# Kernel optimization log

Measured on AMD Instinct MI355X. Metric: run time of the kernel, lower is better.

## Reference

```python
import jax, jax.numpy as jnp
import numpy as np

# DH-SFNN: 2 dendritic LIF layers (denri, no tanh, reset-by-subtraction) + leaky readout integrator.
GAMMA = 0.5   # surrogate gradient scale
LENS = 0.5    # surrogate gradient width
VTH = 1.0     # spike threshold
DT = 1.0

@jax.custom_vjp
def spike_fn(x):
    # Heaviside forward, Gaussian surrogate backward (act_fun_adp)
    return (x > 0.0).astype(x.dtype)

def _spike_fwd(x):
    return spike_fn(x), x

def _spike_bwd(x, g):
    sg = GAMMA * jnp.exp(-x * x / (2.0 * LENS * LENS)) / (jnp.sqrt(2.0 * jnp.pi) * LENS)
    return (g * sg,)

spike_fn.defvjp(_spike_fwd, _spike_bwd)

B, T, IN, H, O, K = 256, 250, 700, 256, 20, 4  # batch, time, in_dim, hidden, out_dim, branch
WARMUP = 10


def _branch_mask(rng, out_dim, in_dim, k):
    # Each neuron's k branches see a disjoint random partition of the inputs.
    m = np.zeros((out_dim * k, in_dim), np.float32)
    step = in_dim // k
    for i in range(out_dim):
        perm = rng.permutation(in_dim)
        for j in range(k):
            m[i * k + j, perm[j * step:(j + 1) * step]] = 1.0
    return m


def setup_inputs() -> dict:
    key = jax.random.key(0)
    ks = jax.random.split(key, 12)
    rng = np.random.default_rng(0)
    s1 = 1.0 / np.sqrt(IN)
    s2 = 1.0 / np.sqrt(H)
    # branch-masked dense weights (apply_mask() already baked in)
    W1 = jax.random.uniform(ks[0], (H * K, IN), minval=-s1, maxval=s1) * jnp.asarray(_branch_mask(rng, H, IN, K))
    b1 = jax.random.uniform(ks[1], (H * K,), minval=-s1, maxval=s1)
    tau_n1 = jax.random.uniform(ks[2], (H, K), minval=2.0, maxval=6.0)
    tau_m1 = jax.random.uniform(ks[3], (H,), minval=0.0, maxval=4.0)
    W2 = jax.random.uniform(ks[4], (H * K, H), minval=-s2, maxval=s2) * jnp.asarray(_branch_mask(rng, H, H, K))
    b2 = jax.random.uniform(ks[5], (H * K,), minval=-s2, maxval=s2)
    tau_n2 = jax.random.uniform(ks[6], (H, K), minval=2.0, maxval=6.0)
    tau_m2 = jax.random.uniform(ks[7], (H,), minval=0.0, maxval=4.0)
    Wr = jax.random.uniform(ks[8], (O, H), minval=-s2, maxval=s2)
    br = jax.random.uniform(ks[9], (O,), minval=-s2, maxval=s2)
    tau_mr = jax.random.uniform(ks[10], (O,), minval=0.0, maxval=4.0)
    # sparse binary spike train input (SHD-like)
    x = (jax.random.uniform(ks[11], (B, T, IN)) < 0.1).astype(jnp.float32)
    return dict(x=x, W1=W1, b1=b1, tau_n1=tau_n1, tau_m1=tau_m1,
                W2=W2, b2=b2, tau_n2=tau_n2, tau_m2=tau_m2,
                Wr=Wr, br=br, tau_mr=tau_mr, warmup=WARMUP)


def reference(x, W1, b1, tau_n1, tau_m1, W2, b2, tau_n2, tau_m2, Wr, br, tau_mr, warmup):
    Bb, Tt, _ = x.shape
    beta1 = jax.nn.sigmoid(tau_n1)   # [H,K] dendritic decay
    alpha1 = jax.nn.sigmoid(tau_m1)  # [H]   soma decay
    beta2 = jax.nn.sigmoid(tau_n2)
    alpha2 = jax.nn.sigmoid(tau_m2)
    alphar = jax.nn.sigmoid(tau_mr)  # [O]

    def dense_branch(inp, W, b):
        return (inp @ W.T + b).reshape(inp.shape[0], -1, K)  # [B,H,K]

    def step(carry, xt):
        d1, m1, s1, d2, m2, s2, mr, acc, t = carry
        # layer 1: dendritic filtering then LIF with soft reset
        d1 = beta1 * d1 + (1.0 - beta1) * dense_branch(xt, W1, b1)
        m1 = m1 * alpha1 + (1.0 - alpha1) * DT * d1.sum(-1) - VTH * s1
        s1 = spike_fn(m1 - VTH)
        # layer 2
        d2 = beta2 * d2 + (1.0 - beta2) * dense_branch(s1, W2, b2)
        m2 = m2 * alpha2 + (1.0 - alpha2) * DT * d2.sum(-1) - VTH * s2
        s2 = spike_fn(m2 - VTH)
        # leaky readout integrator
        mr = mr * alphar + (1.0 - alphar) * (s2 @ Wr.T + br)
        acc = acc + jnp.where(t >= warmup, mr, jnp.zeros_like(mr))
        return (d1, m1, s1, d2, m2, s2, mr, acc, t + 1), None

    z = lambda *s: jnp.zeros(s, x.dtype)
    carry0 = (z(Bb, H, K), z(Bb, H), z(Bb, H),
              z(Bb, H, K), z(Bb, H), z(Bb, H),
              z(Bb, O), z(Bb, O), jnp.int32(0))
    carry, _ = jax.lax.scan(step, carry0, jnp.moveaxis(x, 1, 0))
    acc = carry[7]
    return acc / (Tt - warmup)  # readout_mode == 'mean'
```

## Files before the change

### kernel.cpp

```cpp
#include <hip/hip_runtime.h>
#include <hip/hip_bf16.h>

typedef unsigned short us16;
typedef unsigned int u32;

#define B_   256
#define T_   250
#define IN_  700
#define KP_  704
#define H_   256
#define O_   20
#define HK_  1024
#define NPAIR_ (B_ * T_)
#define LDP_ 40
#define CP_  132

typedef __attribute__((ext_vector_type(8))) short short8;
typedef __attribute__((ext_vector_type(4))) float f32x4;

__device__ __forceinline__ float bfbits(unsigned int lo16) {
    union { unsigned int i; float f; } v; v.i = lo16 << 16; return v.f;
}
__device__ __forceinline__ float bflo(unsigned int u) {
    union { unsigned int i; float f; } v; v.i = u << 16; return v.f;
}
__device__ __forceinline__ float bfhi(unsigned int u) {
    union { unsigned int i; float f; } v; v.i = u & 0xffff0000u; return v.f;
}
__device__ __forceinline__ us16 f2bfu(float f) {
    __hip_bfloat16 h = __float2bfloat16(f);
    union { __hip_bfloat16 h; us16 u; } c; c.h = h; return c.u;
}
__device__ __forceinline__ float sigm(float x) { return 1.0f / (1.0f + expf(-x)); }
__device__ __forceinline__ int rfl(int v) { return __builtin_amdgcn_readfirstlane(v); }

__device__ __forceinline__ bool detect_bf16(const us16* __restrict__ taun) {
    int ok = 0;
#pragma unroll
    for (int i = 0; i < 8; i += 2) ok += ((taun[i] >> 8) == 0x40) ? 1 : 0;
    return ok == 4;
}
__device__ __forceinline__ float ldany(const void* __restrict__ p, long i, bool isb) {
    return isb ? bfbits(((const us16*)p)[i]) : ((const float*)p)[i];
}

__device__ __forceinline__ void async_cp16(const us16* g, us16* l) {
    __builtin_amdgcn_global_load_lds(
        (const __attribute__((address_space(1))) u32*)g,
        (__attribute__((address_space(3))) u32*)l, 16, 0, 0);
}

__global__ __launch_bounds__(256) void cvt_rows2(
    const void* __restrict__ xin, const void* __restrict__ w1in,
    us16* __restrict__ xout, us16* __restrict__ w1out,
    const us16* __restrict__ taun) {
    const bool isb = detect_bf16(taun);
    const int r = blockIdx.x * 4 + (threadIdx.x >> 6);
    const int l = threadIdx.x & 63;
    const void* in; us16* out; long ibase, obase;
    if (r < NPAIR_) {
        in = xin;  out = xout;  ibase = (long)r * IN_; obase = (long)r * KP_;
    } else {
        const int r2 = r - NPAIR_;
        if (r2 >= HK_) return;
        in = w1in; out = w1out; ibase = (long)r2 * IN_; obase = (long)r2 * KP_;
    }
    for (int c = l; c < 176; c += 64) {
        uint2 o;
        if (c < 175) {
            if (isb) {
                o = *(const uint2*)((const us16*)in + ibase + 4 * c);
            } else {
                float4 f = *(const float4*)((const float*)in + ibase + 4 * c);
                o.x = (u32)f2bfu(f.x) | ((u32)f2bfu(f.y) << 16);
                o.y = (u32)f2bfu(f.z) | ((u32)f2bfu(f.w) << 16);
            }
        } else { o.x = 0u; o.y = 0u; }
        *(uint2*)(out + obase + 4 * c) = o;
    }
}

__global__ void transpose_to_bf16(const void* __restrict__ in, us16* __restrict__ out,
                                  int R, int C, const us16* __restrict__ taun) {
    const bool isb = detect_bf16(taun);
    __shared__ us16 tile[32][33];
    int c0 = blockIdx.x * 32, r0 = blockIdx.y * 32;
    int tx = threadIdx.x, ty = threadIdx.y;
#pragma unroll
    for (int j = 0; j < 32; j += 8) {
        int r = r0 + ty + j, c = c0 + tx;
        if (r < R && c < C) tile[ty + j][tx] = f2bfu(ldany(in, (long)r * C + c, isb));
    }
    __syncthreads();
#pragma unroll
    for (int j = 0; j < 32; j += 8) {
        int c = c0 + ty + j, r = r0 + tx;
        if (c < C && r < R) out[(long)c * R + r] = tile[tx][ty + j];
    }
}

__global__ __launch_bounds__(256) void gemm_bf(
    const us16* __restrict__ Xb, const us16* __restrict__ W1b,
    us16* __restrict__ Apre)
{
    __shared__ __align__(16) us16 smem[32768];

    const int L  = blockIdx.x;
    const int mt = (L & 7) + ((L >> 6) << 3);
    const int nt = (L >> 3) & 7;
    if (mt >= NPAIR_ / 128) return;
    const int m0 = mt * 128, n0 = nt * 128;

    const int tid  = threadIdx.x;
    const int lane = tid & 63;
    const int w    = tid >> 6;
    const int wr   = w >> 1, wc = w & 1;
    const int l16  = lane & 15, quad = lane >> 4;

    const int rr    = lane >> 3;
    const int ccsw  = ((lane & 7) ^ rr) * 8;
    const us16* xg[4]; const us16* wg[4];
    int asl[4], bsl[4];
#pragma unroll
    for (int i = 0; i < 4; ++i) {
        const int blkrow = (w * 4 + i) * 8;
        xg[i]  = Xb  + (long)(m0 + blkrow + rr) * KP_ + ccsw;
        wg[i]  = W1b + (long)(n0 + blkrow + rr) * KP_ + ccsw;
        asl[i] = (w * 4 + i) * 512;
        bsl[i] = 8192 + (w * 4 + i) * 512;
    }

    f32x4 acc[4][4];
#pragma unroll
    for (int i = 0; i < 4; ++i)
#pragma unroll
        for (int j = 0; j < 4; ++j) acc[i][j] = (f32x4){0.f, 0.f, 0.f, 0.f};

    const int sw = l16 & 7;
    int aoff0[4], aoff1[4], boff0[4], boff1[4];
#pragma unroll
    for (int i = 0; i < 4; ++i) {
        const int ar = wr * 64 + i * 16 + l16;
        const int br = wc * 64 + i * 16 + l16;
        aoff0[i] = ar * 64 + ((quad ^ sw) << 3);
        aoff1[i] = ar * 64 + (((quad + 4) ^ sw) << 3);
        boff0[i] = 8192 + br * 64 + ((quad ^ sw) << 3);
        boff1[i] = 8192 + br * 64 + (((quad + 4) ^ sw) << 3);
    }

#pragma unroll
    for (int i = 0; i < 4; ++i) async_cp16(xg[i], smem + asl[i]);
#pragma unroll
    for (int i = 0; i < 4; ++i) async_cp16(wg[i], smem + bsl[i]);
    __syncthreads();

    for (int s = 0; s < 11; ++s) {
        const int cur = (s & 1) * 16384;
        const int nxt = 16384 - cur;
        if (s + 1 < 11) {
            const int kb = (s + 1) * 64;
#pragma unroll
            for (int i = 0; i < 4; ++i) async_cp16(xg[i] + kb, smem + nxt + asl[i]);
#pragma unroll
            for (int i = 0; i < 4; ++i) async_cp16(wg[i] + kb, smem + nxt + bsl[i]);
        }

        short8 af[4][2], bfv[4][2];
#pragma unroll
        for (int i = 0; i < 4; ++i) {
            af[i][0]  = *(const short8*)(smem + cur + aoff0[i]);
            af[i][1]  = *(const short8*)(smem + cur + aoff1[i]);
            bfv[i][0] = *(const short8*)(smem + cur + boff0[i]);
            bfv[i][1] = *(const short8*)(smem + cur + boff1[i]);
        }
#pragma unroll
        for (int h = 0; h < 2; ++h)
#pragma unroll
            for (int i = 0; i < 4; ++i)
#pragma unroll
                for (int j = 0; j < 4; ++j)
                    acc[i][j] = __builtin_amdgcn_mfma_f32_16x16x32_bf16(
                        af[i][h], bfv[j][h], acc[i][j], 0, 0, 0);

        __syncthreads();
    }

#pragma unroll
    for (int i = 0; i < 4; ++i)
#pragma unroll
        for (int j = 0; j < 4; ++j)
#pragma unroll
            for (int r = 0; r < 4; ++r)
                smem[(wr * 64 + i * 16 + quad * 4 + r) * CP_ +
                     (wc * 64 + j * 16 + l16)] = f2bfu(acc[i][j][r]);
    __syncthreads();
    for (int r2 = 0; r2 < 32; ++r2) {
        const int row = w * 32 + r2;
        const u32 v = *(const u32*)(smem + row * CP_ + lane * 2);
        *(u32*)(Apre + (long)(m0 + row) * HK_ + n0 + lane * 2) = v;
    }
}

__global__ __launch_bounds__(256) void dhsfnn_pc(
    const us16* __restrict__ Apre,
    const void* __restrict__ b1,  const void* __restrict__ tau_n1,
    const void* __restrict__ tau_m1,
    const void* __restrict__ b2,  const void* __restrict__ tau_n2,
    const void* __restrict__ tau_m2,
    const void* __restrict__ Wr,  const void* __restrict__ br,
    const void* __restrict__ tau_mr,
    const us16* __restrict__ W2T,
    const int* __restrict__ warmup_p,
    void* __restrict__ out)
{
    __shared__ __align__(16) us16 ring[2][16 * HK_];

    const int tid  = threadIdx.x;
    const int lane = tid & 63;
    const int w    = tid >> 6;
    const int b    = blockIdx.x;
    const bool isb = detect_bf16((const us16*)tau_n1);
    const int wu   = *warmup_p;

    const us16* apb = Apre + (long)b * T_ * HK_;

    for (int seg = w; seg < 32; seg += 4)
        async_cp16(apb + seg * 512 + lane * 8, ring[0] + seg * 512);

    float be1[16], cb1[16], ce1[16], be2[16], cb2[16], ce2[16], d1[16], d2[16];
#pragma unroll
    for (int e = 0; e < 16; ++e) {
        const long gi = (e < 8) ? ((long)lane * 8 + e) : (512 + (long)lane * 8 + e - 8);
        const float t1 = sigm(ldany(tau_n1, gi, isb));
        be1[e] = t1; ce1[e] = 1.f - t1; cb1[e] = ce1[e] * ldany(b1, gi, isb);
        const float t2 = sigm(ldany(tau_n2, gi, isb));
        be2[e] = t2; ce2[e] = 1.f - t2; cb2[e] = ce2[e] * ldany(b2, gi, isb);
        d1[e] = 0.f; d2[e] = 0.f;
    }
    float al1[4], al2[4], m1[4], s1[4], m2[4], s2[4];
#pragma unroll
    for (int j = 0; j < 4; ++j) {
        const int n = (j < 2) ? (2 * lane + j) : (128 + 2 * lane + (j - 2));
        al1[j] = sigm(ldany(tau_m1, n, isb));
        al2[j] = sigm(ldany(tau_m2, n, isb));
        m1[j] = 0.f; s1[j] = 0.f; m2[j] = 0.f; s2[j] = 0.f;
    }
    float alr = 0.f, brv = 0.f;
    if (lane < O_) { alr = sigm(ldany(tau_mr, lane, isb)); brv = ldany(br, lane, isb); }
    float mrv = 0.f, accO = 0.f;

    __syncthreads();

    for (int c = 0; c < 16; ++c) {
        const int t0 = c * 16;
        const int nst = (T_ - t0 < 16) ? (T_ - t0) : 16;

        if (w != 0) {
            if (c + 1 < 16) {
                const int t1c  = (c + 1) * 16;
                const int nseg = ((T_ - t1c < 16) ? (T_ - t1c) : 16) * 2;
                const us16* src = apb + (long)t1c * HK_;
                us16* dst = ring[(c + 1) & 1];
                for (int seg = w - 1; seg < nseg; seg += 3)
                    async_cp16(src + seg * 512 + lane * 8, dst + seg * 512);
            }
        } else {
            const us16* rb = ring[c & 1];
            uint4 cLo = *(const uint4*)(rb + lane * 8);
            uint4 cHi = *(const uint4*)(rb + 512 + lane * 8);
            for (int q = 0; q < nst; ++q) {
                uint4 nLo = cLo, nHi = cHi;
                if (q + 1 < nst) {
                    nLo = *(const uint4*)(rb + (q + 1) * HK_ + lane * 8);
                    nHi = *(const uint4*)(rb + (q + 1) * HK_ + 512 + lane * 8);
                }
                const int t = t0 + q;
                float a[16];
                a[0]=bflo(cLo.x);  a[1]=bfhi(cLo.x);  a[2]=bflo(cLo.y);  a[3]=bfhi(cLo.y);
                a[4]=bflo(cLo.z);  a[5]=bfhi(cLo.z);  a[6]=bflo(cLo.w);  a[7]=bfhi(cLo.w);
                a[8]=bflo(cHi.x);  a[9]=bfhi(cHi.x);  a[10]=bflo(cHi.y); a[11]=bfhi(cHi.y);
                a[12]=bflo(cHi.z); a[13]=bfhi(cHi.z); a[14]=bflo(cHi.w); a[15]=bfhi(cHi.w);

#pragma unroll
                for (int e = 0; e < 16; ++e)
                    d1[e] = be1[e] * d1[e] + cb1[e] + ce1[e] * a[e];

                unsigned long long bal1[4];
#pragma unroll
                for (int j = 0; j < 4; ++j) {
                    const float s = (d1[j*4+0] + d1[j*4+1]) + (d1[j*4+2] + d1[j*4+3]);
                    m1[j] = m1[j] * al1[j] + (1.f - al1[j]) * s - s1[j];
                    s1[j] = (m1[j] > 1.0f) ? 1.f : 0.f;
                    bal1[j] = __ballot(s1[j] > 0.f);
                }

                if ((bal1[0] | bal1[1] | bal1[2] | bal1[3]) != 0ull) {
                    float g[16];
#pragma unroll
                    for (int e = 0; e < 16; ++e) g[e] = 0.f;
                    for (int j2 = 0; j2 < 4; ++j2) {
                        unsigned long long mm = bal1[j2];
                        while (mm) {
                            const int i = __ffsll(mm) - 1; mm &= mm - 1;
                            const int n = (j2 < 2) ? (2 * i + j2) : (128 + 2 * i + (j2 - 2));
                            const us16* wv = W2T + ((long)n << 10);
                            const uint4 wl = *(const uint4*)(wv + lane * 8);
                            const uint4 wh = *(const uint4*)(wv + 512 + lane * 8);
                            g[0]+=bflo(wl.x);  g[1]+=bfhi(wl.x);  g[2]+=bflo(wl.y);  g[3]+=bfhi(wl.y);
                            g[4]+=bflo(wl.z);  g[5]+=bfhi(wl.z);  g[6]+=bflo(wl.w);  g[7]+=bfhi(wl.w);
                            g[8]+=bflo(wh.x);  g[9]+=bfhi(wh.x);  g[10]+=bflo(wh.y); g[11]+=bfhi(wh.y);
                            g[12]+=bflo(wh.z); g[13]+=bfhi(wh.z); g[14]+=bflo(wh.w); g[15]+=bfhi(wh.w);
                        }
                    }
#pragma unroll
                    for (int e = 0; e < 16; ++e)
                        d2[e] = be2[e] * d2[e] + cb2[e] + ce2[e] * g[e];
                } else {
#pragma unroll
                    for (int e = 0; e < 16; ++e)
                        d2[e] = be2[e] * d2[e] + cb2[e];
                }

                unsigned long long bal2[4];
#pragma unroll
                for (int j = 0; j < 4; ++j) {
                    const float s = (d2[j*4+0] + d2[j*4+1]) + (d2[j*4+2] + d2[j*4+3]);
                    m2[j] = m2[j] * al2[j] + (1.f - al2[j]) * s - s2[j];
                    s2[j] = (m2[j] > 1.0f) ? 1.f : 0.f;
                    bal2[j] = __ballot(s2[j] > 0.f);
                }

                if (lane < O_) {
                    float sum = brv;
                    if ((bal2[0] | bal2[1] | bal2[2] | bal2[3]) != 0ull) {
                        for (int j2 = 0; j2 < 4; ++j2) {
                            unsigned long long mm = bal2[j2];
                            while (mm) {
                                const int i = __ffsll(mm) - 1; mm &= mm - 1;
                                const int n = (j2 < 2) ? (2 * i + j2) : (128 + 2 * i + (j2 - 2));
                                sum += ldany(Wr, (long)lane * H_ + n, isb);
                            }
                        }
                    }
                    mrv = alr * mrv + (1.f - alr) * sum;
                    if (t >= wu) accO += mrv;
                }
                cLo = nLo; cHi = nHi;
            }
        }
        __syncthreads();
    }

    if (w == 0 && lane < O_) {
        const float res = accO / (float)(T_ - wu);
        if (isb) ((us16*)out)[b * O_ + lane] = f2bfu(res);
        else     ((float*)out)[b * O_ + lane] = res;
    }
}

#define GA_LOAD(S, AV, BV) do {                                               \
    const int k0_ = (S) * 32 + half16;                                        \
    if (k0_ + 16 <= IN_) {                                                    \
        if (isb) {                                                            \
            const us16* pa_ = (const us16*)X  + arow + k0_;                   \
            const us16* pb_ = (const us16*)W1 + brow + k0_;                   \
            uint2 a0_ = *(const uint2*)pa_,        a1_ = *(const uint2*)(pa_ + 4);  \
            uint2 a2_ = *(const uint2*)(pa_ + 8),  a3_ = *(const uint2*)(pa_ + 12); \
            uint2 b0_ = *(const uint2*)pb_,        b1_ = *(const uint2*)(pb_ + 4);  \
            uint2 b2_ = *(const uint2*)(pb_ + 8),  b3_ = *(const uint2*)(pb_ + 12); \
            AV[0]=a0_.x; AV[1]=a0_.y; AV[2]=a1_.x; AV[3]=a1_.y;               \
            AV[4]=a2_.x; AV[5]=a2_.y; AV[6]=a3_.x; AV[7]=a3_.y;               \
            BV[0]=b0_.x; BV[1]=b0_.y; BV[2]=b1_.x; BV[3]=b1_.y;               \
            BV[4]=b2_.x; BV[5]=b2_.y; BV[6]=b3_.x; BV[7]=b3_.y;               \
        } else {                                                              \
            const float* pa_ = (const float*)X  + arow + k0_;                 \
            const float* pb_ = (const float*)W1 + brow + k0_;                 \
            float4 fa0_ = *(const float4*)pa_,        fa1_ = *(const float4*)(pa_ + 4);  \
            float4 fa2_ = *(const float4*)(pa_ + 8),  fa3_ = *(const float4*)(pa_ + 12); \
            float4 fb0_ = *(const float4*)pb_,        fb1_ = *(const float4*)(pb_ + 4);  \
            float4 fb2_ = *(const float4*)(pb_ + 8),  fb3_ = *(const float4*)(pb_ + 12); \
            AV[0] = (unsigned)f2bfu(fa0_.x) | ((unsigned)f2bfu(fa0_.y) << 16); \
            AV[1] = (unsigned)f2bfu(fa0_.z) | ((unsigned)f2bfu(fa0_.w) << 16); \
            AV[2] = (unsigned)f2bfu(fa1_.x) | ((unsigned)f2bfu(fa1_.y) << 16); \
            AV[3] = (unsigned)f2bfu(fa1_.z) | ((unsigned)f2bfu(fa1_.w) << 16); \
            AV[4] = (unsigned)f2bfu(fa2_.x) | ((unsigned)f2bfu(fa2_.y) << 16); \
            AV[5] = (unsigned)f2bfu(fa2_.z) | ((unsigned)f2bfu(fa2_.w) << 16); \
            AV[6] = (unsigned)f2bfu(fa3_.x) | ((unsigned)f2bfu(fa3_.y) << 16); \
            AV[7] = (unsigned)f2bfu(fa3_.z) | ((unsigned)f2bfu(fa3_.w) << 16); \
            BV[0] = (unsigned)f2bfu(fb0_.x) | ((unsigned)f2bfu(fb0_.y) << 16); \
            BV[1] = (unsigned)f2bfu(fb0_.z) | ((unsigned)f2bfu(fb0_.w) << 16); \
            BV[2] = (unsigned)f2bfu(fb1_.x) | ((unsigned)f2bfu(fb1_.y) << 16); \
            BV[3] = (unsigned)f2bfu(fb1_.z) | ((unsigned)f2bfu(fb1_.w) << 16); \
            BV[4] = (unsigned)f2bfu(fb2_.x) | ((unsigned)f2bfu(fb2_.y) << 16); \
            BV[5] = (unsigned)f2bfu(fb2_.z) | ((unsigned)f2bfu(fb2_.w) << 16); \
            BV[6] = (unsigned)f2bfu(fb3_.x) | ((unsigned)f2bfu(fb3_.y) << 16); \
            BV[7] = (unsigned)f2bfu(fb3_.z) | ((unsigned)f2bfu(fb3_.w) << 16); \
        }                                                                     \
    } else {                                                                  \
        _Pragma("unroll")                                                     \
        for (int e_ = 0; e_ < 8; ++e_) { AV[e_] = 0u; BV[e_] = 0u; }          \
        _Pragma("unroll")                                                     \
        for (int e_ = 0; e_ < 16; ++e_) {                                     \
            int k_ = k0_ + e_;                                                \
            if (k_ < IN_) {                                                   \
                unsigned va_ = (unsigned)f2bfu(ldany(X,  arow + k_, isb));    \
                unsigned vb_ = (unsigned)f2bfu(ldany(W1, brow + k_, isb));    \
                AV[e_ >> 1] |= va_ << ((e_ & 1) * 16);                        \
                BV[e_ >> 1] |= vb_ << ((e_ & 1) * 16);                        \
            }                                                                 \
        }                                                                     \
    }                                                                         \
} while (0)

#define GA_STORE(AV, BV) do {                                                 \
    uint4 u0_; u0_.x = AV[0]; u0_.y = AV[1]; u0_.z = AV[2]; u0_.w = AV[3];    \
    uint4 u1_; u1_.x = AV[4]; u1_.y = AV[5]; u1_.z = AV[6]; u1_.w = AV[7];    \
    uint4 v0_; v0_.x = BV[0]; v0_.y = BV[1]; v0_.z = BV[2]; v0_.w = BV[3];    \
    uint4 v1_; v1_.x = BV[4]; v1_.y = BV[5]; v1_.z = BV[6]; v1_.w = BV[7];    \
    *(uint4*)asw       = u0_; *(uint4*)(asw + 8) = u1_;                       \
    *(uint4*)bsw       = v0_; *(uint4*)(bsw + 8) = v1_;                       \
} while (0)

#define GA_MFMA() do {                                                        \
    short8 af_[4], bf_[4];                                                    \
    _Pragma("unroll")                                                         \
    for (int i_ = 0; i_ < 4; ++i_) af_[i_] = *(const short8*)(As + aoff[i_]); \
    _Pragma("unroll")                                                         \
    for (int j_ = 0; j_ < 4; ++j_) bf_[j_] = *(const short8*)(Bs + boff[j_]); \
    _Pragma("unroll")                                                         \
    for (int i_ = 0; i_ < 4; ++i_)                                            \
        _Pragma("unroll")                                                     \
        for (int j_ = 0; j_ < 4; ++j_)                                        \
            acc[i_][j_] = __builtin_amdgcn_mfma_f32_16x16x32_bf16(            \
                af_[i_], bf_[j_], acc[i_][j_], 0, 0, 0);                      \
} while (0)

__global__ __launch_bounds__(256) void gemm_apre(
    const void* __restrict__ X, const void* __restrict__ W1,
    const us16* __restrict__ taun, us16* __restrict__ Apre)
{
    const bool isb = detect_bf16(taun);
    __shared__ __align__(16) us16 As[128 * LDP_];
    __shared__ __align__(16) us16 Bs[128 * LDP_];

    const int L  = blockIdx.x;
    const int mt = (L & 7) + ((L >> 6) << 3);
    const int nt = (L >> 3) & 7;
    if (mt >= NPAIR_ / 128) return;
    const int m0 = mt * 128, n0 = nt * 128;

    const int tid  = threadIdx.x;
    const int lane = tid & 63;
    const int w    = tid >> 6;
    const int wr   = w >> 1, wc = w & 1;
    const int l16  = lane & 15, quad = lane >> 4;
    const int ra   = tid >> 1;
    const int half16 = (tid & 1) * 16;

    f32x4 acc[4][4];
#pragma unroll
    for (int i = 0; i < 4; ++i)
#pragma unroll
        for (int j = 0; j < 4; ++j) acc[i][j] = (f32x4){0.f, 0.f, 0.f, 0.f};

    int aoff[4], boff[4];
#pragma unroll
    for (int i = 0; i < 4; ++i) {
        aoff[i] = (wr * 64 + i * 16 + l16) * LDP_ + quad * 8;
        boff[i] = (wc * 64 + i * 16 + l16) * LDP_ + quad * 8;
    }

    const long arow = (long)(m0 + ra) * IN_;
    const long brow = (long)(n0 + ra) * IN_;
    us16* asw = As + ra * LDP_ + half16;
    us16* bsw = Bs + ra * LDP_ + half16;

    unsigned av0[8], bv0[8], av1[8], bv1[8];
    GA_LOAD(0, av0, bv0);

    for (int ss = 0; ss < 11; ++ss) {
        __syncthreads();
        GA_STORE(av0, bv0);
        __syncthreads();
        GA_LOAD(2 * ss + 1, av1, bv1);
        GA_MFMA();
        __syncthreads();
        GA_STORE(av1, bv1);
        __syncthreads();
        if (ss < 10) GA_LOAD(2 * ss + 2, av0, bv0);
        GA_MFMA();
    }

#pragma unroll
    for (int i = 0; i < 4; ++i) {
#pragma unroll
        for (int j = 0; j < 4; ++j) {
            const int gm = m0 + wr * 64 + i * 16 + quad * 4;
            const int gn = n0 + wc * 64 + j * 16 + l16;
            us16* op = Apre + (long)gm * HK_ + gn;
#pragma unroll
            for (int r = 0; r < 4; ++r)
                op[(long)r * HK_] = f2bfu(acc[i][j][r]);
        }
    }
}

__global__ __launch_bounds__(64) void dhsfnn_wave(
    const us16* __restrict__ Apre,
    const void* __restrict__ b1,  const void* __restrict__ tau_n1,
    const void* __restrict__ tau_m1,
    const void* __restrict__ b2,  const void* __restrict__ tau_n2,
    const void* __restrict__ tau_m2,
    const void* __restrict__ Wr,  const void* __restrict__ br,
    const void* __restrict__ tau_mr,
    const us16* __restrict__ W2T,
    const int* __restrict__ warmup_p,
    void* __restrict__ out)
{
    const int lane = threadIdx.x;
    const int b    = blockIdx.x;
    const bool isb = detect_bf16((const us16*)tau_n1);
    const int wu   = *warmup_p;

    float be1[16], cb1[16], be2[16], cb2[16], d1[16], d2[16];
#pragma unroll
    for (int e = 0; e < 16; ++e) {
        const long gi = (long)lane * 16 + e;
        const float t1 = sigm(ldany(tau_n1, gi, isb));
        be1[e] = t1; cb1[e] = (1.f - t1) * ldany(b1, gi, isb);
        const float t2 = sigm(ldany(tau_n2, gi, isb));
        be2[e] = t2; cb2[e] = (1.f - t2) * ldany(b2, gi, isb);
        d1[e] = 0.f; d2[e] = 0.f;
    }
    float al1[4], al2[4], m1[4], s1[4], m2[4], s2[4];
#pragma unroll
    for (int j = 0; j < 4; ++j) {
        al1[j] = sigm(ldany(tau_m1, lane * 4 + j, isb));
        al2[j] = sigm(ldany(tau_m2, lane * 4 + j, isb));
        m1[j] = 0.f; s1[j] = 0.f; m2[j] = 0.f; s2[j] = 0.f;
    }
    float alr = 0.f, brv = 0.f;
    if (lane < O_) { alr = sigm(ldany(tau_mr, lane, isb)); brv = ldany(br, lane, isb); }
    float mrv = 0.f, accO = 0.f;

    const us16* ap = Apre + (long)b * T_ * HK_ + lane * 16;

    auto wstep = [&](int t, uint4 lo, uint4 hi) {
        float a[16];
        a[0]=bflo(lo.x);  a[1]=bfhi(lo.x);  a[2]=bflo(lo.y);  a[3]=bfhi(lo.y);
        a[4]=bflo(lo.z);  a[5]=bfhi(lo.z);  a[6]=bflo(lo.w);  a[7]=bfhi(lo.w);
        a[8]=bflo(hi.x);  a[9]=bfhi(hi.x);  a[10]=bflo(hi.y); a[11]=bfhi(hi.y);
        a[12]=bflo(hi.z); a[13]=bfhi(hi.z); a[14]=bflo(hi.w); a[15]=bfhi(hi.w);
#pragma unroll
        for (int e = 0; e < 16; ++e)
            d1[e] = be1[e] * d1[e] + cb1[e] + (1.f - be1[e]) * a[e];
        unsigned long long bal1[4];
#pragma unroll
        for (int j = 0; j < 4; ++j) {
            const float s = (d1[j*4+0] + d1[j*4+1]) + (d1[j*4+2] + d1[j*4+3]);
            m1[j] = m1[j] * al1[j] + (1.f - al1[j]) * s - s1[j];
            s1[j] = (m1[j] > 1.0f) ? 1.f : 0.f;
            bal1[j] = __ballot(s1[j] > 0.f);
        }
        if ((bal1[0] | bal1[1] | bal1[2] | bal1[3]) != 0ull) {
            float g[16];
#pragma unroll
            for (int e = 0; e < 16; ++e) g[e] = 0.f;
            for (int j2 = 0; j2 < 4; ++j2) {
                unsigned long long mm = bal1[j2];
                while (mm) {
                    const int i = __ffsll(mm) - 1; mm &= mm - 1;
                    const us16* wv = W2T + ((long)(i * 4 + j2) << 10) + lane * 16;
                    const uint4 wl = *(const uint4*)wv;
                    const uint4 wh = *(const uint4*)(wv + 8);
                    g[0]+=bflo(wl.x);  g[1]+=bfhi(wl.x);  g[2]+=bflo(wl.y);  g[3]+=bfhi(wl.y);
                    g[4]+=bflo(wl.z);  g[5]+=bfhi(wl.z);  g[6]+=bflo(wl.w);  g[7]+=bfhi(wl.w);
                    g[8]+=bflo(wh.x);  g[9]+=bfhi(wh.x);  g[10]+=bflo(wh.y); g[11]+=bfhi(wh.y);
                    g[12]+=bflo(wh.z); g[13]+=bfhi(wh.z); g[14]+=bflo(wh.w); g[15]+=bfhi(wh.w);
                }
            }
#pragma unroll
            for (int e = 0; e < 16; ++e)
                d2[e] = be2[e] * d2[e] + cb2[e] + (1.f - be2[e]) * g[e];
        } else {
#pragma unroll
            for (int e = 0; e < 16; ++e)
                d2[e] = be2[e] * d2[e] + cb2[e];
        }
        unsigned long long bal2[4];
#pragma unroll
        for (int j = 0; j < 4; ++j) {
            const float s = (d2[j*4+0] + d2[j*4+1]) + (d2[j*4+2] + d2[j*4+3]);
            m2[j] = m2[j] * al2[j] + (1.f - al2[j]) * s - s2[j];
            s2[j] = (m2[j] > 1.0f) ? 1.f : 0.f;
            bal2[j] = __ballot(s2[j] > 0.f);
        }
        if (lane < O_) {
            float sum = brv;
            if ((bal2[0] | bal2[1] | bal2[2] | bal2[3]) != 0ull) {
                for (int j2 = 0; j2 < 4; ++j2) {
                    unsigned long long mm = bal2[j2];
                    while (mm) {
                        const int i = __ffsll(mm) - 1; mm &= mm - 1;
                        sum += ldany(Wr, (long)lane * H_ + (i * 4 + j2), isb);
                    }
                }
            }
            mrv = alr * mrv + (1.f - alr) * sum;
            if (t >= wu) accO += mrv;
        }
    };

    uint4 q0a = *(const uint4*)(ap);
    uint4 q0b = *(const uint4*)(ap + 8);
    uint4 q1a = *(const uint4*)(ap + HK_);
    uint4 q1b = *(const uint4*)(ap + HK_ + 8);
    uint4 q2a = *(const uint4*)(ap + 2 * HK_);
    uint4 q2b = *(const uint4*)(ap + 2 * HK_ + 8);
    uint4 q3a = *(const uint4*)(ap + 3 * HK_);
    uint4 q3b = *(const uint4*)(ap + 3 * HK_ + 8);

    int t = 0;
    for (int it = 0; it < 62; ++it) {
        wstep(t + 0, q0a, q0b);
        q0a = *(const uint4*)(ap + (long)(t + 4) * HK_);
        q0b = *(const uint4*)(ap + (long)(t + 4) * HK_ + 8);
        wstep(t + 1, q1a, q1b);
        if (t + 5 < T_) {
            q1a = *(const uint4*)(ap + (long)(t + 5) * HK_);
            q1b = *(const uint4*)(ap + (long)(t + 5) * HK_ + 8);
        }
        wstep(t + 2, q2a, q2b);
        if (t + 6 < T_) {
            q2a = *(const uint4*)(ap + (long)(t + 6) * HK_);
            q2b = *(const uint4*)(ap + (long)(t + 6) * HK_ + 8);
        }
        wstep(t + 3, q3a, q3b);
        if (t + 7 < T_) {
            q3a = *(const uint4*)(ap + (long)(t + 7) * HK_);
            q3b = *(const uint4*)(ap + (long)(t + 7) * HK_ + 8);
        }
        t += 4;
    }
    wstep(248, q0a, q0b);
    wstep(249, q1a, q1b);

    if (lane < O_) {
        const float res = accO / (float)(T_ - wu);
        if (isb) ((us16*)out)[b * O_ + lane] = f2bfu(res);
        else     ((float*)out)[b * O_ + lane] = res;
    }
}

__global__ __launch_bounds__(256) void dhsfnn_fb(
    const void* __restrict__ x,  const void* __restrict__ W1,
    const void* __restrict__ b1, const void* __restrict__ tau_n1,
    const void* __restrict__ tau_m1,
    const void* __restrict__ W2, const void* __restrict__ b2,
    const void* __restrict__ tau_n2, const void* __restrict__ tau_m2,
    const void* __restrict__ Wr, const void* __restrict__ br,
    const void* __restrict__ tau_mr,
    const int* __restrict__ warmup_p,
    void* __restrict__ out)
{
    __shared__ us16 list1[1024];
    __shared__ us16 list2[256];
    __shared__ us16 list3[256];
    __shared__ int n1s, n2s, n3s;

    const int tid = threadIdx.x;
    const int b   = blockIdx.x;
    const int h   = tid;
    const bool isb = detect_bf16((const us16*)tau_n1);
    const int wu  = *warmup_p;

    const float be1_0 = sigm(ldany(tau_n1, 4 * h + 0, isb));
    const float be1_1 = sigm(ldany(tau_n1, 4 * h + 1, isb));
    const float be1_2 = sigm(ldany(tau_n1, 4 * h + 2, isb));
    const float be1_3 = sigm(ldany(tau_n1, 4 * h + 3, isb));
    const float bi1_0 = ldany(b1, 4 * h + 0, isb), bi1_1 = ldany(b1, 4 * h + 1, isb);
    const float bi1_2 = ldany(b1, 4 * h + 2, isb), bi1_3 = ldany(b1, 4 * h + 3, isb);
    const float al1 = sigm(ldany(tau_m1, h, isb));
    const float be2_0 = sigm(ldany(tau_n2, 4 * h + 0, isb));
    const float be2_1 = sigm(ldany(tau_n2, 4 * h + 1, isb));
    const float be2_2 = sigm(ldany(tau_n2, 4 * h + 2, isb));
    const float be2_3 = sigm(ldany(tau_n2, 4 * h + 3, isb));
    const float bi2_0 = ldany(b2, 4 * h + 0, isb), bi2_1 = ldany(b2, 4 * h + 1, isb);
    const float bi2_2 = ldany(b2, 4 * h + 2, isb), bi2_3 = ldany(b2, 4 * h + 3, isb);
    const float al2 = sigm(ldany(tau_m2, h, isb));
    float alr = 0.f, brv = 0.f;
    if (h < O_) { alr = sigm(ldany(tau_mr, h, isb)); brv = ldany(br, h, isb); }

    float d1_0 = 0.f, d1_1 = 0.f, d1_2 = 0.f, d1_3 = 0.f, m1v = 0.f, s1f = 0.f;
    float d2_0 = 0.f, d2_1 = 0.f, d2_2 = 0.f, d2_3 = 0.f, m2v = 0.f, s2f = 0.f;
    float mrv = 0.f, accO = 0.f;

    const long xbase = (long)b * T_ * IN_;
    float xv0 = ldany(x, xbase + tid, isb);
    float xv1 = ldany(x, xbase + tid + 256, isb);
    float xv2 = (tid + 512 < IN_) ? ldany(x, xbase + tid + 512, isb) : 0.f;

    for (int t = 0; t < T_; ++t) {
        const bool p0 = xv0 != 0.f, p1 = xv1 != 0.f, p2 = xv2 != 0.f;
        if (t + 1 < T_) {
            const long nbx = xbase + (long)(t + 1) * IN_;
            xv0 = ldany(x, nbx + tid, isb);
            xv1 = ldany(x, nbx + tid + 256, isb);
            xv2 = (tid + 512 < IN_) ? ldany(x, nbx + tid + 512, isb) : 0.f;
        }
        __syncthreads();
        if (tid == 0) { n1s = 0; n2s = 0; n3s = 0; }
        __syncthreads();
        if (p0) { int p = atomicAdd(&n1s, 1); list1[p & 1023] = (us16)tid; }
        if (p1) { int p = atomicAdd(&n1s, 1); list1[p & 1023] = (us16)(tid + 256); }
        if (p2) { int p = atomicAdd(&n1s, 1); list1[p & 1023] = (us16)(tid + 512); }
        __syncthreads();
        int n1 = n1s; n1 = (n1 < 1024) ? n1 : 1024;

        float a0 = 0.f, a1 = 0.f, a2 = 0.f, a3 = 0.f;
#pragma unroll 2
        for (int idx = 0; idx < n1; ++idx) {
            int i = rfl((int)list1[idx]);
            i = (i < IN_) ? i : (IN_ - 1);
            long r = (long)(h * 4) * IN_ + i;
            a0 += ldany(W1, r, isb);
            a1 += ldany(W1, r + IN_, isb);
            a2 += ldany(W1, r + 2 * IN_, isb);
            a3 += ldany(W1, r + 3 * IN_, isb);
        }
        d1_0 = be1_0 * d1_0 + (1.f - be1_0) * (bi1_0 + a0);
        d1_1 = be1_1 * d1_1 + (1.f - be1_1) * (bi1_1 + a1);
        d1_2 = be1_2 * d1_2 + (1.f - be1_2) * (bi1_2 + a2);
        d1_3 = be1_3 * d1_3 + (1.f - be1_3) * (bi1_3 + a3);
        m1v = m1v * al1 + (1.f - al1) * (d1_0 + d1_1 + d1_2 + d1_3) - s1f;
        s1f = (m1v > 1.0f) ? 1.f : 0.f;

        if (s1f > 0.f) { int p = atomicAdd(&n2s, 1); list2[p & 255] = (us16)tid; }
        __syncthreads();
        int n2 = n2s; n2 = (n2 < 256) ? n2 : 256;

        a0 = 0.f; a1 = 0.f; a2 = 0.f; a3 = 0.f;
#pragma unroll 2
        for (int idx = 0; idx < n2; ++idx) {
            int i = rfl((int)list2[idx]);
            i = (i < H_) ? i : (H_ - 1);
            long r = (long)(h * 4) * H_ + i;
            a0 += ldany(W2, r, isb);
            a1 += ldany(W2, r + H_, isb);
            a2 += ldany(W2, r + 2 * H_, isb);
            a3 += ldany(W2, r + 3 * H_, isb);
        }
        d2_0 = be2_0 * d2_0 + (1.f - be2_0) * (bi2_0 + a0);
        d2_1 = be2_1 * d2_1 + (1.f - be2_1) * (bi2_1 + a1);
        d2_2 = be2_2 * d2_2 + (1.f - be2_2) * (bi2_2 + a2);
        d2_3 = be2_3 * d2_3 + (1.f - be2_3) * (bi2_3 + a3);
        m2v = m2v * al2 + (1.f - al2) * (d2_0 + d2_1 + d2_2 + d2_3) - s2f;
        s2f = (m2v > 1.0f) ? 1.f : 0.f;

        if (s2f > 0.f) { int p = atomicAdd(&n3s, 1); list3[p & 255] = (us16)tid; }
        __syncthreads();
        int n3 = n3s; n3 = (n3 < 256) ? n3 : 256;

        if (h < O_) {
            float sum = brv;
            for (int idx = 0; idx < n3; ++idx) {
                int j = (int)list3[idx];
                j = (j < H_) ? j : (H_ - 1);
                sum += ldany(Wr, (long)h * H_ + j, isb);
            }
            mrv = alr * mrv + (1.f - alr) * sum;
            if (t >= wu) accO += mrv;
        }
    }
    if (h < O_) {
        float res = accO / (float)(T_ - wu);
        if (isb) ((us16*)out)[b * O_ + h] = f2bfu(res);
        else     ((float*)out)[b * O_ + h] = res;
    }
}

extern "C" void kernel_launch(void* const* d_in, const int* in_sizes, int n_in,
                              void* d_out, int out_size, void* d_ws, size_t ws_size,
                              hipStream_t stream) {
    const void* x      = d_in[0];
    const void* W1     = d_in[1];
    const void* b1     = d_in[2];
    const void* tau_n1 = d_in[3];
    const void* tau_m1 = d_in[4];
    const void* W2     = d_in[5];
    const void* b2     = d_in[6];
    const void* tau_n2 = d_in[7];
    const void* tau_m2 = d_in[8];
    const void* Wr     = d_in[9];
    const void* br     = d_in[10];
    const void* tau_mr = d_in[11];
    const int*  warmup = (const int*)d_in[12];

    const size_t w2t_bytes  = (size_t)H_ * HK_ * 2;
    const size_t xbf_bytes  = (size_t)NPAIR_ * KP_ * 2;
    const size_t w1b_bytes  = (size_t)HK_ * KP_ * 2;
    const size_t apre_bytes = (size_t)NPAIR_ * HK_ * 2;

    const bool tier0 = (d_ws != nullptr &&
                        ws_size >= w2t_bytes + xbf_bytes + w1b_bytes + apre_bytes);
    const bool tier1 = (d_ws != nullptr && ws_size >= w2t_bytes + apre_bytes);

    dim3 blk(32, 8);
    if (tier0) {
        us16* W2T  = (us16*)d_ws;
        us16* Xbf  = (us16*)((char*)d_ws + w2t_bytes);
        us16* W1bf = (us16*)((char*)d_ws + w2t_bytes + xbf_bytes);
        us16* Apre = (us16*)((char*)d_ws + w2t_bytes + xbf_bytes + w1b_bytes);
        cvt_rows2<<<(NPAIR_ + HK_) / 4, 256, 0, stream>>>(
            x, W1, Xbf, W1bf, (const us16*)tau_n1);
        transpose_to_bf16<<<dim3((H_ + 31) / 32, (HK_ + 31) / 32), blk, 0, stream>>>(
            W2, W2T, HK_, H_, (const us16*)tau_n1);
        gemm_bf<<<4096, 256, 0, stream>>>(Xbf, W1bf, Apre);
        dhsfnn_pc<<<B_, 256, 0, stream>>>(
            Apre, b1, tau_n1, tau_m1, b2, tau_n2, tau_m2,
            Wr, br, tau_mr, W2T, warmup, d_out);
    } else if (tier1) {
        us16* W2T  = (us16*)d_ws;
        us16* Apre = (us16*)((char*)d_ws + w2t_bytes);
        transpose_to_bf16<<<dim3((H_ + 31) / 32, (HK_ + 31) / 32), blk, 0, stream>>>(
            W2, W2T, HK_, H_, (const us16*)tau_n1);
        gemm_apre<<<4096, 256, 0, stream>>>(x, W1, (const us16*)tau_n1, Apre);
        dhsfnn_wave<<<B_, 64, 0, stream>>>(
            Apre, b1, tau_n1, tau_m1, b2, tau_n2, tau_m2,
            Wr, br, tau_mr, W2T, warmup, d_out);
    } else {
        dhsfnn_fb<<<B_, 256, 0, stream>>>(x, W1, b1, tau_n1, tau_m1,
                                          W2, b2, tau_n2, tau_m2,
                                          Wr, br, tau_mr, warmup, d_out);
    }
}
```

Before: 455.3 us.

## Fuse conversion, GEMM and recurrence into one cooperative persistent kernel

Replaces the four-kernel pipeline (bf16 conversion, W2 transpose, input GEMM, recurrent scan) with a single cooperative kernel of 512 blocks that runs each phase in turn, separated by grid-wide syncs. The aim is to remove launch gaps and tail effects between the stages. The recurrence phase uses only 256 of the 512 blocks and puts compute in one wave while three waves prefetch Apre into an LDS ring. This may be slower than the dedicated dhsfnn_pc kernel, and the launch bound of 2 blocks per CU limits registers. If the cooperative launch fails, it falls back to the old path.

```diff
diff --git a/kernel.cpp b/kernel.cpp
--- a/kernel.cpp
+++ b/kernel.cpp
@@ -1,5 +1,8 @@
 #include <hip/hip_runtime.h>
 #include <hip/hip_bf16.h>
+#include <hip/hip_cooperative_groups.h>
+
+namespace cg = cooperative_groups;
 
 typedef unsigned short us16;
 typedef unsigned int u32;
@@ -48,6 +51,295 @@
     __builtin_amdgcn_global_load_lds(
         (const __attribute__((address_space(1))) u32*)g,
         (__attribute__((address_space(3))) u32*)l, 16, 0, 0);
+}
+
+__global__ __launch_bounds__(256, 2) void dhsfnn_mega(
+    const void* __restrict__ x,  const void* __restrict__ W1,
+    const void* __restrict__ W2, const void* __restrict__ Wr,
+    const void* __restrict__ b1, const void* __restrict__ tau_n1,
+    const void* __restrict__ tau_m1,
+    const void* __restrict__ b2, const void* __restrict__ tau_n2,
+    const void* __restrict__ tau_m2,
+    const void* __restrict__ br, const void* __restrict__ tau_mr,
+    const int* __restrict__ warmup_p,
+    us16* __restrict__ Xbf, us16* __restrict__ W1bf,
+    us16* __restrict__ W2T, us16* __restrict__ Apre,
+    void* __restrict__ out)
+{
+    cg::grid_group grid = cg::this_grid();
+    __shared__ __align__(16) us16 smem[32768];
+
+    const int tid  = threadIdx.x;
+    const int lane = tid & 63;
+    const int w    = tid >> 6;
+    const bool isb = detect_bf16((const us16*)tau_n1);
+
+    for (int r = blockIdx.x * 4 + w; r < NPAIR_ + HK_; r += 2048) {
+        const void* in; us16* outp; long ibase, obase;
+        if (r < NPAIR_) {
+            in = x;  outp = Xbf;  ibase = (long)r * IN_; obase = (long)r * KP_;
+        } else {
+            const int r2 = r - NPAIR_;
+            in = W1; outp = W1bf; ibase = (long)r2 * IN_; obase = (long)r2 * KP_;
+        }
+        for (int c = lane; c < 176; c += 64) {
+            uint2 o;
+            if (c < 175) {
+                if (isb) {
+                    o = *(const uint2*)((const us16*)in + ibase + 4 * c);
+                } else {
+                    float4 f = *(const float4*)((const float*)in + ibase + 4 * c);
+                    o.x = (u32)f2bfu(f.x) | ((u32)f2bfu(f.y) << 16);
+                    o.y = (u32)f2bfu(f.z) | ((u32)f2bfu(f.w) << 16);
+                }
+            } else { o.x = 0u; o.y = 0u; }
+            *(uint2*)(outp + obase + 4 * c) = o;
+        }
+    }
+    for (int e = blockIdx.x * 256 + tid; e < H_ * HK_; e += 512 * 256) {
+        const int c = e >> 10, n = e & (HK_ - 1);
+        W2T[e] = f2bfu(ldany(W2, (long)n * H_ + c, isb));
+    }
+    grid.sync();
+
+    {
+        const int wr   = w >> 1, wc = w & 1;
+        const int l16  = lane & 15, quad = lane >> 4;
+        const int rr   = lane >> 3;
+        const int ccsw = ((lane & 7) ^ rr) * 8;
+        const int sw   = l16 & 7;
+
+        int aoff0[4], aoff1[4], boff0[4], boff1[4];
+#pragma unroll
+        for (int i = 0; i < 4; ++i) {
+            const int ar = wr * 64 + i * 16 + l16;
+            const int br2 = wc * 64 + i * 16 + l16;
+            aoff0[i] = ar * 64 + ((quad ^ sw) << 3);
+            aoff1[i] = ar * 64 + (((quad + 4) ^ sw) << 3);
+            boff0[i] = 8192 + br2 * 64 + ((quad ^ sw) << 3);
+            boff1[i] = 8192 + br2 * 64 + (((quad + 4) ^ sw) << 3);
+        }
+
+        for (int L = blockIdx.x; L < 4096; L += 512) {
+            const int mt = (L & 7) + ((L >> 6) << 3);
+            const int nt = (L >> 3) & 7;
+            if (mt >= NPAIR_ / 128) continue;
+            const int m0 = mt * 128, n0 = nt * 128;
+
+            const us16* xg[4]; const us16* wg[4];
+            int asl[4], bsl[4];
+#pragma unroll
+            for (int i = 0; i < 4; ++i) {
+                const int blkrow = (w * 4 + i) * 8;
+                xg[i]  = Xbf  + (long)(m0 + blkrow + rr) * KP_ + ccsw;
+                wg[i]  = W1bf + (long)(n0 + blkrow + rr) * KP_ + ccsw;
+                asl[i] = (w * 4 + i) * 512;
+                bsl[i] = 8192 + (w * 4 + i) * 512;
+            }
+
+            f32x4 acc[4][4];
+#pragma unroll
+            for (int i = 0; i < 4; ++i)
+#pragma unroll
+                for (int j = 0; j < 4; ++j) acc[i][j] = (f32x4){0.f, 0.f, 0.f, 0.f};
+
+#pragma unroll
+            for (int i = 0; i < 4; ++i) async_cp16(xg[i], smem + asl[i]);
+#pragma unroll
+            for (int i = 0; i < 4; ++i) async_cp16(wg[i], smem + bsl[i]);
+            __syncthreads();
+
+            for (int s = 0; s < 11; ++s) {
+                const int cur = (s & 1) * 16384;
+                const int nxt = 16384 - cur;
+                if (s + 1 < 11) {
+                    const int kb = (s + 1) * 64;
+#pragma unroll
+                    for (int i = 0; i < 4; ++i) async_cp16(xg[i] + kb, smem + nxt + asl[i]);
+#pragma unroll
+                    for (int i = 0; i < 4; ++i) async_cp16(wg[i] + kb, smem + nxt + bsl[i]);
+                }
+
+                short8 af[4][2], bfv[4][2];
+#pragma unroll
+                for (int i = 0; i < 4; ++i) {
+                    af[i][0]  = *(const short8*)(smem + cur + aoff0[i]);
+                    af[i][1]  = *(const short8*)(smem + cur + aoff1[i]);
+                    bfv[i][0] = *(const short8*)(smem + cur + boff0[i]);
+                    bfv[i][1] = *(const short8*)(smem + cur + boff1[i]);
+                }
+#pragma unroll
+                for (int h = 0; h < 2; ++h)
+#pragma unroll
+                    for (int i = 0; i < 4; ++i)
+#pragma unroll
+                        for (int j = 0; j < 4; ++j)
+                            acc[i][j] = __builtin_amdgcn_mfma_f32_16x16x32_bf16(
+                                af[i][h], bfv[j][h], acc[i][j], 0, 0, 0);
+
+                __syncthreads();
+            }
+
+#pragma unroll
+            for (int i = 0; i < 4; ++i)
+#pragma unroll
+                for (int j = 0; j < 4; ++j)
+#pragma unroll
+                    for (int r = 0; r < 4; ++r)
+                        smem[(wr * 64 + i * 16 + quad * 4 + r) * CP_ +
+                             (wc * 64 + j * 16 + l16)] = f2bfu(acc[i][j][r]);
+            __syncthreads();
+            for (int r2 = 0; r2 < 32; ++r2) {
+                const int row = w * 32 + r2;
+                const u32 v = *(const u32*)(smem + row * CP_ + lane * 2);
+                *(u32*)(Apre + (long)(m0 + row) * HK_ + n0 + lane * 2) = v;
+            }
+            __syncthreads();
+        }
+    }
+    grid.sync();
+
+    if (blockIdx.x < B_) {
+        us16* ring0 = smem;
+        us16* ring1 = smem + 16 * HK_;
+        const int b  = blockIdx.x;
+        const int wu = *warmup_p;
+
+        const us16* apb = Apre + (long)b * T_ * HK_;
+
+        for (int seg = w; seg < 32; seg += 4)
+            async_cp16(apb + seg * 512 + lane * 8, ring0 + seg * 512);
+
+        float be1[16], cb1[16], ce1[16], be2[16], cb2[16], ce2[16], d1[16], d2[16];
+#pragma unroll
+        for (int e = 0; e < 16; ++e) {
+            const long gi = (e < 8) ? ((long)lane * 8 + e) : (512 + (long)lane * 8 + e - 8);
+            const float t1 = sigm(ldany(tau_n1, gi, isb));
+            be1[e] = t1; ce1[e] = 1.f - t1; cb1[e] = ce1[e] * ldany(b1, gi, isb);
+            const float t2 = sigm(ldany(tau_n2, gi, isb));
+            be2[e] = t2; ce2[e] = 1.f - t2; cb2[e] = ce2[e] * ldany(b2, gi, isb);
+            d1[e] = 0.f; d2[e] = 0.f;
+        }
+        float al1[4], al2[4], m1[4], s1[4], m2[4], s2[4];
+#pragma unroll
+        for (int j = 0; j < 4; ++j) {
+            const int n = (j < 2) ? (2 * lane + j) : (128 + 2 * lane + (j - 2));
+            al1[j] = sigm(ldany(tau_m1, n, isb));
+            al2[j] = sigm(ldany(tau_m2, n, isb));
+            m1[j] = 0.f; s1[j] = 0.f; m2[j] = 0.f; s2[j] = 0.f;
+        }
+        float alr = 0.f, brv = 0.f;
+        if (lane < O_) { alr = sigm(ldany(tau_mr, lane, isb)); brv = ldany(br, lane, isb); }
+        float mrv = 0.f, accO = 0.f;
+
+        __syncthreads();
+
+        for (int c = 0; c < 16; ++c) {
+            const int t0 = c * 16;
+            const int nst = (T_ - t0 < 16) ? (T_ - t0) : 16;
+
+            if (w != 0) {
+                if (c + 1 < 16) {
+                    const int t1c  = (c + 1) * 16;
+                    const int nseg = ((T_ - t1c < 16) ? (T_ - t1c) : 16) * 2;
+                    const us16* src = apb + (long)t1c * HK_;
+                    us16* dst = ((c + 1) & 1) ? ring1 : ring0;
+                    for (int seg = w - 1; seg < nseg; seg += 3)
+                        async_cp16(src + seg * 512 + lane * 8, dst + seg * 512);
+                }
+            } else {
+                const us16* rb = (c & 1) ? ring1 : ring0;
+                uint4 cLo = *(const uint4*)(rb + lane * 8);
+                uint4 cHi = *(const uint4*)(rb + 512 + lane * 8);
+                for (int q = 0; q < nst; ++q) {
+                    uint4 nLo = cLo, nHi = cHi;
+                    if (q + 1 < nst) {
+                        nLo = *(const uint4*)(rb + (q + 1) * HK_ + lane * 8);
+                        nHi = *(const uint4*)(rb + (q + 1) * HK_ + 512 + lane * 8);
+                    }
+                    const int t = t0 + q;
+                    float a[16];
+                    a[0]=bflo(cLo.x);  a[1]=bfhi(cLo.x);  a[2]=bflo(cLo.y);  a[3]=bfhi(cLo.y);
+                    a[4]=bflo(cLo.z);  a[5]=bfhi(cLo.z);  a[6]=bflo(cLo.w);  a[7]=bfhi(cLo.w);
+                    a[8]=bflo(cHi.x);  a[9]=bfhi(cHi.x);  a[10]=bflo(cHi.y); a[11]=bfhi(cHi.y);
+                    a[12]=bflo(cHi.z); a[13]=bfhi(cHi.z); a[14]=bflo(cHi.w); a[15]=bfhi(cHi.w);
+
+#pragma unroll
+                    for (int e = 0; e < 16; ++e)
+                        d1[e] = be1[e] * d1[e] + cb1[e] + ce1[e] * a[e];
+
+                    unsigned long long bal1[4];
+#pragma unroll
+                    for (int j = 0; j < 4; ++j) {
+                        const float s = (d1[j*4+0] + d1[j*4+1]) + (d1[j*4+2] + d1[j*4+3]);
+                        m1[j] = m1[j] * al1[j] + (1.f - al1[j]) * s - s1[j];
+                        s1[j] = (m1[j] > 1.0f) ? 1.f : 0.f;
+                        bal1[j] = __ballot(s1[j] > 0.f);
+                    }
+
+                    if ((bal1[0] | bal1[1] | bal1[2] | bal1[3]) != 0ull) {
+                        float g[16];
+#pragma unroll
+                        for (int e = 0; e < 16; ++e) g[e] = 0.f;
+                        for (int j2 = 0; j2 < 4; ++j2) {
+                            unsigned long long mm = bal1[j2];
+                            while (mm) {
+                                const int i = __ffsll(mm) - 1; mm &= mm - 1;
+                                const int n = (j2 < 2) ? (2 * i + j2) : (128 + 2 * i + (j2 - 2));
+                                const us16* wv = W2T + ((long)n << 10);
+                                const uint4 wl = *(const uint4*)(wv + lane * 8);
+                                const uint4 wh = *(const uint4*)(wv + 512 + lane * 8);
+                                g[0]+=bflo(wl.x);  g[1]+=bfhi(wl.x);  g[2]+=bflo(wl.y);  g[3]+=bfhi(wl.y);
+                                g[4]+=bflo(wl.z);  g[5]+=bfhi(wl.z);  g[6]+=bflo(wl.w);  g[7]+=bfhi(wl.w);
+                                g[8]+=bflo(wh.x);  g[9]+=bfhi(wh.x);  g[10]+=bflo(wh.y); g[11]+=bfhi(wh.y);
+                                g[12]+=bflo(wh.z); g[13]+=bfhi(wh.z); g[14]+=bflo(wh.w); g[15]+=bfhi(wh.w);
+                            }
+                        }
+#pragma unroll
+                        for (int e = 0; e < 16; ++e)
+                            d2[e] = be2[e] * d2[e] + cb2[e] + ce2[e] * g[e];
+                    } else {
+#pragma unroll
+                        for (int e = 0; e < 16; ++e)
+                            d2[e] = be2[e] * d2[e] + cb2[e];
+                    }
+
+                    unsigned long long bal2[4];
+#pragma unroll
+                    for (int j = 0; j < 4; ++j) {
+                        const float s = (d2[j*4+0] + d2[j*4+1]) + (d2[j*4+2] + d2[j*4+3]);
+                        m2[j] = m2[j] * al2[j] + (1.f - al2[j]) * s - s2[j];
+                        s2[j] = (m2[j] > 1.0f) ? 1.f : 0.f;
+                        bal2[j] = __ballot(s2[j] > 0.f);
+                    }
+
+                    if (lane < O_) {
+                        float sum = brv;
+                        if ((bal2[0] | bal2[1] | bal2[2] | bal2[3]) != 0ull) {
+                            for (int j2 = 0; j2 < 4; ++j2) {
+                                unsigned long long mm = bal2[j2];
+                                while (mm) {
+                                    const int i = __ffsll(mm) - 1; mm &= mm - 1;
+                                    const int n = (j2 < 2) ? (2 * i + j2) : (128 + 2 * i + (j2 - 2));
+                                    sum += ldany(Wr, (long)lane * H_ + n, isb);
+                                }
+                            }
+                        }
+                        mrv = alr * mrv + (1.f - alr) * sum;
+                        if (t >= wu) accO += mrv;
+                    }
+                    cLo = nLo; cHi = nHi;
+                }
+            }
+            __syncthreads();
+        }
+
+        if (w == 0 && lane < O_) {
+            const float res = accO / (float)(T_ - wu);
+            if (isb) ((us16*)out)[b * O_ + lane] = f2bfu(res);
+            else     ((float*)out)[b * O_ + lane] = res;
+        }
+    }
 }
 
 __global__ __launch_bounds__(256) void cvt_rows2(
@@ -811,14 +1103,28 @@
         us16* Xbf  = (us16*)((char*)d_ws + w2t_bytes);
         us16* W1bf = (us16*)((char*)d_ws + w2t_bytes + xbf_bytes);
         us16* Apre = (us16*)((char*)d_ws + w2t_bytes + xbf_bytes + w1b_bytes);
-        cvt_rows2<<<(NPAIR_ + HK_) / 4, 256, 0, stream>>>(
-            x, W1, Xbf, W1bf, (const us16*)tau_n1);
-        transpose_to_bf16<<<dim3((H_ + 31) / 32, (HK_ + 31) / 32), blk, 0, stream>>>(
-            W2, W2T, HK_, H_, (const us16*)tau_n1);
-        gemm_bf<<<4096, 256, 0, stream>>>(Xbf, W1bf, Apre);
-        dhsfnn_pc<<<B_, 256, 0, stream>>>(
-            Apre, b1, tau_n1, tau_m1, b2, tau_n2, tau_m2,
-            Wr, br, tau_mr, W2T, warmup, d_out);
+
+        void* args[] = {
+            (void*)&x,  (void*)&W1, (void*)&W2, (void*)&Wr,
+            (void*)&b1, (void*)&tau_n1, (void*)&tau_m1,
+            (void*)&b2, (void*)&tau_n2, (void*)&tau_m2,
+            (void*)&br, (void*)&tau_mr, (void*)&warmup,
+            (void*)&Xbf, (void*)&W1bf, (void*)&W2T, (void*)&Apre,
+            (void*)&d_out
+        };
+        hipError_t ce = hipLaunchCooperativeKernel(
+            (const void*)dhsfnn_mega, dim3(512), dim3(256), args, 0, stream);
+        if (ce != hipSuccess) {
+            (void)hipGetLastError();
+            cvt_rows2<<<(NPAIR_ + HK_) / 4, 256, 0, stream>>>(
+                x, W1, Xbf, W1bf, (const us16*)tau_n1);
+            transpose_to_bf16<<<dim3((H_ + 31) / 32, (HK_ + 31) / 32), blk, 0, stream>>>(
+                W2, W2T, HK_, H_, (const us16*)tau_n1);
+            gemm_bf<<<4096, 256, 0, stream>>>(Xbf, W1bf, Apre);
+            dhsfnn_pc<<<B_, 256, 0, stream>>>(
+                Apre, b1, tau_n1, tau_m1, b2, tau_n2, tau_m2,
+                Wr, br, tau_mr, W2T, warmup, d_out);
+        }
     } else if (tier1) {
         us16* W2T  = (us16*)d_ws;
         us16* Apre = (us16*)((char*)d_ws + w2t_bytes);
```

After: 621.6 us. 1.37x slower.
